# Kernel optimization log

Measured on AMD Instinct MI355X. Metric: run time of the kernel, lower is better.

Reference implementation:

```python
import jax, jax.numpy as jnp
import numpy as np
from jax import lax

D_TEMPORAL, D_INNER, D_STATE, D_CONV, DT_RANK = 2, 4, 16, 4, 1
EPS = 1e-5


def setup_inputs() -> dict:
    key = jax.random.key(0)
    ks = jax.random.split(key, 14)
    B, L = 16, 32768
    f = lambda k, s, scale=1.0: jax.random.normal(k, s, jnp.float32) * scale
    dt_b = float(np.log(np.expm1(0.01)))  # softplus^-1(0.01), typical dt init
    A_log = jnp.log(jnp.tile(jnp.arange(1, D_STATE + 1, dtype=jnp.float32), (D_INNER, 1)))
    return {
        "hidden_states": f(ks[0], (B, D_TEMPORAL, L)),
        "norm_w": jnp.ones((D_TEMPORAL,), jnp.float32),
        "in_proj_w": f(ks[1], (2 * D_INNER, D_TEMPORAL), 0.5),
        "conv_w": f(ks[2], (D_INNER, D_CONV), 0.3),
        "conv_b": f(ks[3], (D_INNER,), 0.1),
        "x_proj_w": f(ks[4], (DT_RANK + 2 * D_STATE, D_INNER), 0.3),
        "dt_proj_w": f(ks[5], (D_INNER, DT_RANK), 1.0),
        "dt_proj_b": jnp.full((D_INNER,), dt_b, jnp.float32),
        "A_log": A_log,
        "D": jnp.ones((D_INNER,), jnp.float32),
        "conv_w_b": f(ks[6], (D_INNER, D_CONV), 0.3),
        "conv_b_b": f(ks[7], (D_INNER,), 0.1),
        "x_proj_w_b": f(ks[8], (DT_RANK + 2 * D_STATE, D_INNER), 0.3),
        "dt_proj_w_b": f(ks[9], (D_INNER, DT_RANK), 1.0),
        "dt_proj_b_b": jnp.full((D_INNER,), dt_b, jnp.float32),
        "A_b_log": A_log,
        "D_b": jnp.ones((D_INNER,), jnp.float32),
        "out_proj_w": f(ks[10], (D_TEMPORAL, D_INNER), 0.3),
        "norm_f_w": jnp.ones((D_TEMPORAL,), jnp.float32),
    }


def _silu(x):
    return x * jax.nn.sigmoid(x)


def _rmsnorm(x, w):
    return x * lax.rsqrt(jnp.mean(x * x, axis=-1, keepdims=True) + EPS) * w


def _branch(x, z, conv_w, conv_b, x_proj_w, dt_proj_w, dt_proj_b, A_log, D):
    # x, z: (B, d_inner, L). Causal depthwise conv + silu.
    Bb, d, L = x.shape
    xc = lax.conv_general_dilated(
        x, conv_w[:, None, :], (1,), [(D_CONV - 1, 0)],
        feature_group_count=d, dimension_numbers=("NCH", "OIH", "NCH"))
    u = _silu(xc + conv_b[None, :, None]).transpose(0, 2, 1)      # (B, L, d)
    x_dbl = u @ x_proj_w.T                                        # (B, L, rank+2n)
    dt, Bm, Cm = jnp.split(x_dbl, [DT_RANK, DT_RANK + D_STATE], axis=-1)
    dt = jax.nn.softplus(dt @ dt_proj_w.T + dt_proj_b)            # (B, L, d)
    A = -jnp.exp(A_log)                                           # (d, n)
    dA = jnp.exp(dt[..., None] * A)                               # (B, L, d, n)
    dBu = (dt * u)[..., None] * Bm[:, :, None, :]                 # (B, L, d, n)

    def step(h, inp):
        dA_t, dBu_t, C_t = inp
        h = dA_t * h + dBu_t                                      # (B, d, n)
        return h, jnp.einsum("bdn,bn->bd", h, C_t)

    h0 = jnp.zeros((Bb, d, D_STATE), dtype=u.dtype)
    _, ys = lax.scan(step, h0, (jnp.swapaxes(dA, 0, 1), jnp.swapaxes(dBu, 0, 1), jnp.swapaxes(Cm, 0, 1)))
    y = jnp.swapaxes(ys, 0, 1) + u * D                            # (B, L, d)
    return y * _silu(z.transpose(0, 2, 1))


def _forward(hidden_states, norm_w, in_proj_w, conv_w, conv_b, x_proj_w, dt_proj_w,
             dt_proj_b, A_log, D, conv_w_b, conv_b_b, x_proj_w_b, dt_proj_w_b,
             dt_proj_b_b, A_b_log, D_b, out_proj_w, norm_f_w):
    # hidden_states: (B, T=d_temporal, L); scan runs over L.
    hs = jnp.swapaxes(hidden_states, 1, 2)                        # (B, L, T)
    residual = hs.astype(jnp.float32)
    hs = _rmsnorm(residual, norm_w)
    xz = jnp.swapaxes(hs @ in_proj_w.T, 1, 2)                     # (B, 2*d_inner, L)
    x, z = jnp.split(xz, 2, axis=1)
    y_f = _branch(x, z, conv_w, conv_b, x_proj_w, dt_proj_w, dt_proj_b, A_log, D)
    y_b = _branch(x[..., ::-1], z[..., ::-1], conv_w_b, conv_b_b, x_proj_w_b,
                  dt_proj_w_b, dt_proj_b_b, A_b_log, D_b)
    y = y_f + y_b[:, ::-1, :]                                     # (B, L, d_inner)
    out = y @ out_proj_w.T                                        # (B, L, T)
    out = _rmsnorm(out + residual, norm_f_w)
    return jnp.swapaxes(out, 1, 2)                                # (B, T, L)


def reference(hidden_states, norm_w, in_proj_w, conv_w, conv_b, x_proj_w, dt_proj_w,
              dt_proj_b, A_log, D, conv_w_b, conv_b_b, x_proj_w_b, dt_proj_w_b,
              dt_proj_b_b, A_b_log, D_b, out_proj_w, norm_f_w):
    return _forward(hidden_states, norm_w, in_proj_w, conv_w, conv_b, x_proj_w,
                    dt_proj_w, dt_proj_b, A_log, D, conv_w_b, conv_b_b, x_proj_w_b,
                    dt_proj_w_b, dt_proj_b_b, A_b_log, D_b, out_proj_w, norm_f_w)
```

## Files before the change

### kernel.cpp

```cpp
#include <hip/hip_runtime.h>
#include <hip/hip_bf16.h>
#include <cstdint>

#define BB 16
#define LL 32768
#define NC 512

#define WD_SZ 256
#define XPW 0
#define CVW 132
#define CVB 148
#define DTW 152
#define DTB 156
#define AW  160
#define DW  224
#define G_INPROJ 512
#define G_NORMW 528
#define G_OUTP 530
#define G_NORMF 538
#define FLG 1000

#define PQ_OFF 4096
#define PQ_BYTES ((size_t)BB*2*NC*64*8)
#define HIN_OFF (PQ_OFF + PQ_BYTES)
#define HIN_BYTES ((size_t)BB*2*NC*64*4)
#define PLN_OFF (HIN_OFF + HIN_BYTES)
#define PLN_STRIDE 14336
#define PLN_BYTES ((size_t)BB*NC*PLN_STRIDE)

#define O_DTF 0
#define O_DTB 1088
#define O_DUF 2176
#define O_DUB 2752
#define O_BCF 3328
#define O_BCB 7680
#define O_ZS  12032
#define O_UD  13056

__device__ __forceinline__ float bf2f(unsigned short u){ return __uint_as_float(((unsigned int)u)<<16); }
__device__ __forceinline__ float blo(unsigned int u){ return __uint_as_float(u<<16); }
__device__ __forceinline__ float bhi(unsigned int u){ return __uint_as_float(u & 0xffff0000u); }
__device__ __forceinline__ unsigned short f2bf(float f){
  unsigned int x = __float_as_uint(f);
  x += 0x7fffu + ((x>>16)&1u);
  return (unsigned short)(x>>16);
}
__device__ __forceinline__ unsigned int pack2(float a, float b){
  __hip_bfloat162 h = __float22bfloat162_rn(make_float2(a,b));
  union { __hip_bfloat162 h2; unsigned int u; } cv; cv.h2 = h;
  return cv.u;
}
__device__ __forceinline__ float siluf(float x){
  return x * __builtin_amdgcn_rcpf(1.f + __expf(-x));
}
__device__ __forceinline__ float softplusf_(float x){
  return fmaxf(x,0.f) + 0.69314718056f*__log2f(1.f + __expf(-fabsf(x)));
}

__device__ __forceinline__ float rowsum16(float x){
  union { float f; int i; } a, t;
  a.f = x;
  t.i = __builtin_amdgcn_update_dpp(0, a.i, 0x121, 0xf, 0xf, true); a.f += t.f;
  t.i = __builtin_amdgcn_update_dpp(0, a.i, 0x122, 0xf, 0xf, true); a.f += t.f;
  t.i = __builtin_amdgcn_update_dpp(0, a.i, 0x124, 0xf, 0xf, true); a.f += t.f;
  t.i = __builtin_amdgcn_update_dpp(0, a.i, 0x128, 0xf, 0xf, true); a.f += t.f;
  return a.f;
}

__device__ __forceinline__ float ldw(const void* p, int i, int isf){
  return isf ? ((const float*)p)[i] : bf2f(((const unsigned short*)p)[i]);
}
__device__ __forceinline__ float2 hid2(const void* hid, int isf, int b, int t){
  if (isf){
    const float* p = (const float*)hid;
    return make_float2(p[(size_t)b*2*LL + t], p[(size_t)b*2*LL + LL + t]);
  }
  const unsigned short* p = (const unsigned short*)hid;
  return make_float2(bf2f(p[(size_t)b*2*LL + t]), bf2f(p[(size_t)b*2*LL + LL + t]));
}
__device__ __forceinline__ float4 xrow(const void* __restrict__ hid, int isf,
                                       const float* __restrict__ W, int b, int t){
  float2 h = hid2(hid, isf, b, t);
  float ms = rsqrtf(0.5f*(h.x*h.x + h.y*h.y) + 1e-5f);
  float v0 = h.x*ms*W[G_NORMW], v1 = h.y*ms*W[G_NORMW+1];
  float4 x;
  x.x = W[G_INPROJ+0]*v0 + W[G_INPROJ+1]*v1;
  x.y = W[G_INPROJ+2]*v0 + W[G_INPROJ+3]*v1;
  x.z = W[G_INPROJ+4]*v0 + W[G_INPROJ+5]*v1;
  x.w = W[G_INPROJ+6]*v0 + W[G_INPROJ+7]*v1;
  return x;
}

__device__ __forceinline__ void phaseA(const void* __restrict__ hid, int isf,
    const float* __restrict__ W, int b, int c, int lane,
    unsigned char* smem, float4* xb)
{
  float* dtF = (float*)(smem+O_DTF);
  float* dtB = (float*)(smem+O_DTB);
  unsigned short* duF = (unsigned short*)(smem+O_DUF);
  unsigned short* duB = (unsigned short*)(smem+O_DUB);
  unsigned int* BCF = (unsigned int*)(smem+O_BCF);
  unsigned int* BCB = (unsigned int*)(smem+O_BCB);
  float* zsP = (float*)(smem+O_ZS);
  float* uDP = (float*)(smem+O_UD);
  {
    int t = c*64 + lane;
    float2 h = hid2(hid, isf, b, t);
    float ms = rsqrtf(0.5f*(h.x*h.x + h.y*h.y) + 1e-5f);
    float v0 = h.x*ms*W[G_NORMW], v1 = h.y*ms*W[G_NORMW+1];
    float4 x;
    x.x = W[G_INPROJ+0]*v0 + W[G_INPROJ+1]*v1;
    x.y = W[G_INPROJ+2]*v0 + W[G_INPROJ+3]*v1;
    x.z = W[G_INPROJ+4]*v0 + W[G_INPROJ+5]*v1;
    x.w = W[G_INPROJ+6]*v0 + W[G_INPROJ+7]*v1;
    xb[lane+3] = x;
    float4 z4;
    z4.x = siluf(W[G_INPROJ+ 8]*v0 + W[G_INPROJ+ 9]*v1);
    z4.y = siluf(W[G_INPROJ+10]*v0 + W[G_INPROJ+11]*v1);
    z4.z = siluf(W[G_INPROJ+12]*v0 + W[G_INPROJ+13]*v1);
    z4.w = siluf(W[G_INPROJ+14]*v0 + W[G_INPROJ+15]*v1);
    *(float4*)&zsP[lane*4] = z4;
    if (lane < 3){
      int t2 = c*64 - 3 + lane;
      float4 v = make_float4(0.f,0.f,0.f,0.f);
      if (t2 >= 0) v = xrow(hid, isf, W, b, t2);
      xb[lane] = v;
    }
    if (lane >= 61){
      int t3 = c*64 + lane + 3;
      float4 v = make_float4(0.f,0.f,0.f,0.f);
      if (t3 < LL) v = xrow(hid, isf, W, b, t3);
      xb[lane+6] = v;
    }
  }
  __syncthreads();
  float4 xk0=xb[lane],xk1=xb[lane+1],xk2=xb[lane+2],xk3=xb[lane+3];
  float4 xk4=xb[lane+4],xk5=xb[lane+5],xk6=xb[lane+6];
  float uf[4], ub[4];
  uf[0] = siluf(W[CVB+0] + W[CVW+ 0]*xk0.x + W[CVW+ 1]*xk1.x + W[CVW+ 2]*xk2.x + W[CVW+ 3]*xk3.x);
  uf[1] = siluf(W[CVB+1] + W[CVW+ 4]*xk0.y + W[CVW+ 5]*xk1.y + W[CVW+ 6]*xk2.y + W[CVW+ 7]*xk3.y);
  uf[2] = siluf(W[CVB+2] + W[CVW+ 8]*xk0.z + W[CVW+ 9]*xk1.z + W[CVW+10]*xk2.z + W[CVW+11]*xk3.z);
  uf[3] = siluf(W[CVB+3] + W[CVW+12]*xk0.w + W[CVW+13]*xk1.w + W[CVW+14]*xk2.w + W[CVW+15]*xk3.w);
  const float* Wb = W + WD_SZ;
  ub[0] = siluf(Wb[CVB+0] + Wb[CVW+ 0]*xk6.x + Wb[CVW+ 1]*xk5.x + Wb[CVW+ 2]*xk4.x + Wb[CVW+ 3]*xk3.x);
  ub[1] = siluf(Wb[CVB+1] + Wb[CVW+ 4]*xk6.y + Wb[CVW+ 5]*xk5.y + Wb[CVW+ 6]*xk4.y + Wb[CVW+ 7]*xk3.y);
  ub[2] = siluf(Wb[CVB+2] + Wb[CVW+ 8]*xk6.z + Wb[CVW+ 9]*xk5.z + Wb[CVW+10]*xk4.z + Wb[CVW+11]*xk3.z);
  ub[3] = siluf(Wb[CVB+3] + Wb[CVW+12]*xk6.w + Wb[CVW+13]*xk5.w + Wb[CVW+14]*xk4.w + Wb[CVW+15]*xk3.w);
  *(float4*)&uDP[lane*4] = make_float4(
      uf[0]*W[DW+0]+ub[0]*Wb[DW+0], uf[1]*W[DW+1]+ub[1]*Wb[DW+1],
      uf[2]*W[DW+2]+ub[2]*Wb[DW+2], uf[3]*W[DW+3]+ub[3]*Wb[DW+3]);
  #pragma unroll
  for (int dr=0; dr<2; dr++){
    const float* Wd = W + dr*WD_SZ;
    const float* uu = dr ? ub : uf;
    float* dtp = dr ? dtB : dtF;
    unsigned short* dup = dr ? duB : duF;
    unsigned int* bcp = dr ? BCB : BCF;
    float dtr = Wd[XPW+0]*uu[0]+Wd[XPW+1]*uu[1]+Wd[XPW+2]*uu[2]+Wd[XPW+3]*uu[3];
    #pragma unroll
    for (int d2=0; d2<4; d2++){
      float dt = softplusf_(fmaf(Wd[DTW+d2], dtr, Wd[DTB+d2]));
      dtp[d2*68+lane] = dt;
      dup[d2*72+lane] = f2bf(dt*uu[d2]);
    }
    #pragma unroll
    for (int n=0;n<16;n++){
      float Bn = Wd[XPW+(1+n)*4+0]*uu[0]+Wd[XPW+(1+n)*4+1]*uu[1]
               + Wd[XPW+(1+n)*4+2]*uu[2]+Wd[XPW+(1+n)*4+3]*uu[3];
      float Cn = Wd[XPW+(17+n)*4+0]*uu[0]+Wd[XPW+(17+n)*4+1]*uu[1]
               + Wd[XPW+(17+n)*4+2]*uu[2]+Wd[XPW+(17+n)*4+3]*uu[3];
      bcp[n*68+lane] = pack2(Bn,Cn);
    }
  }
}

__global__ void k_prep(const void* __restrict__ normw, const void* __restrict__ inpj,
    const void* __restrict__ cwf, const void* __restrict__ cbf,
    const void* __restrict__ xpf, const void* __restrict__ dwf,
    const void* __restrict__ dbf, const void* __restrict__ alf,
    const void* __restrict__ ddf,
    const void* __restrict__ cwb, const void* __restrict__ cbb,
    const void* __restrict__ xpb, const void* __restrict__ dwb,
    const void* __restrict__ dbb, const void* __restrict__ alb,
    const void* __restrict__ ddb,
    const void* __restrict__ outp, const void* __restrict__ nfw,
    float* __restrict__ W)
{
  const int isf = (((const unsigned int*)ddf)[0] == 0x3F800000u) ? 1 : 0;
  int t = threadIdx.x;
  for (int i=t;i<132;i+=256){ W[XPW+i]=ldw(xpf,i,isf); W[WD_SZ+XPW+i]=ldw(xpb,i,isf); }
  for (int i=t;i<16;i+=256){ W[CVW+i]=ldw(cwf,i,isf); W[WD_SZ+CVW+i]=ldw(cwb,i,isf); W[G_INPROJ+i]=ldw(inpj,i,isf); }
  for (int i=t;i<4;i+=256){
    W[CVB+i]=ldw(cbf,i,isf); W[WD_SZ+CVB+i]=ldw(cbb,i,isf);
    W[DTW+i]=ldw(dwf,i,isf); W[WD_SZ+DTW+i]=ldw(dwb,i,isf);
    W[DTB+i]=ldw(dbf,i,isf); W[WD_SZ+DTB+i]=ldw(dbb,i,isf);
    W[DW+i] =ldw(ddf,i,isf); W[WD_SZ+DW+i] =ldw(ddb,i,isf);
  }
  for (int i=t;i<64;i+=256){
    W[AW+i]       = -__expf(ldw(alf,i,isf)) * 1.44269504089f;
    W[WD_SZ+AW+i] = -__expf(ldw(alb,i,isf)) * 1.44269504089f;
  }
  for (int i=t;i<8;i+=256) W[G_OUTP+i]=ldw(outp,i,isf);
  for (int i=t;i<2;i+=256){ W[G_NORMW+i]=ldw(normw,i,isf); W[G_NORMF+i]=ldw(nfw,i,isf); }
  if (t==0) W[FLG] = (float)isf;
}

template<bool SPL>
__global__ __launch_bounds__(64) void k_chunk(const void* __restrict__ hid,
    const float* __restrict__ W, float2* __restrict__ PQ,
    unsigned char* __restrict__ planes)
{
  __shared__ __align__(16) unsigned char smem[PLN_STRIDE];
  __shared__ __align__(16) float4 xb[70];
  const int lane = threadIdx.x;
  const int gid  = blockIdx.x;
  const int c    = gid & (NC-1);
  const int b    = gid >> 9;
  const int isf  = (int)W[FLG];

  phaseA(hid, isf, W, b, c, lane, smem, xb);
  __syncthreads();
  if (SPL){
    uint4* gp = (uint4*)(planes + (size_t)gid*PLN_STRIDE);
    const uint4* sp = (const uint4*)smem;
    #pragma unroll
    for (int i=0;i<14;i++) gp[i*64+lane] = sp[i*64+lane];
  }
  const float* dtF = (const float*)(smem+O_DTF);
  const float* dtB = (const float*)(smem+O_DTB);
  const unsigned short* duF = (const unsigned short*)(smem+O_DUF);
  const unsigned short* duB = (const unsigned short*)(smem+O_DUB);
  const unsigned int* BCF = (const unsigned int*)(smem+O_BCF);
  const unsigned int* BCB = (const unsigned int*)(smem+O_BCB);
  const int d = lane>>4, n = lane&15;
  const float Af = W[AW + d*16 + n];
  const float Ab = W[WD_SZ + AW + d*16 + n];
  float Pf=1.f, Qf=0.f, Pb=1.f, Qb=0.f;
  for (int j4=0; j4<16; j4++){
    const int t0f = j4*4, t0b = 60 - j4*4;
    float4 df4 = *(const float4*)&dtF[d*68+t0f];
    float4 db4 = *(const float4*)&dtB[d*68+t0b];
    uint2 uf2 = *(const uint2*)&duF[d*72+t0f];
    uint2 ub2 = *(const uint2*)&duB[d*72+t0b];
    uint4 cf4 = *(const uint4*)&BCF[n*68+t0f];
    uint4 cb4 = *(const uint4*)&BCB[n*68+t0b];
    float dfa[4]={df4.x,df4.y,df4.z,df4.w}, dba[4]={db4.x,db4.y,db4.z,db4.w};
    float duf[4]={blo(uf2.x),bhi(uf2.x),blo(uf2.y),bhi(uf2.y)};
    float dub[4]={blo(ub2.x),bhi(ub2.x),blo(ub2.y),bhi(ub2.y)};
    unsigned int cfa[4]={cf4.x,cf4.y,cf4.z,cf4.w}, cba[4]={cb4.x,cb4.y,cb4.z,cb4.w};
    #pragma unroll
    for (int jr=0; jr<4; jr++){
      float e = exp2f(Af*dfa[jr]);
      Pf *= e;
      Qf = fmaf(Qf, e, duf[jr]*blo(cfa[jr]));
      const int k = 3-jr;
      float eb = exp2f(Ab*dba[k]);
      Pb *= eb;
      Qb = fmaf(Qb, eb, dub[k]*blo(cba[k]));
    }
  }
  PQ[((size_t)(b*2+0)*NC + c)*64 + lane]        = make_float2(Pf,Qf);
  PQ[((size_t)(b*2+1)*NC + (NC-1-c))*64 + lane] = make_float2(Pb,Qb);
}

__global__ __launch_bounds__(256) void k_scan(const float2* __restrict__ PQ, float* __restrict__ hin)
{
  __shared__ float2 seg[4][64];
  const int bd = blockIdx.x;
  const int lane = threadIdx.x & 63;
  const int w = threadIdx.x >> 6;
  const size_t base = (size_t)bd*NC;
  const int c0 = w*128;
  float h = 0.f, R = 1.f;
  for (int cc=0; cc<128; cc+=16){
    float2 v[16];
    #pragma unroll
    for (int k=0;k<16;k++) v[k] = PQ[(base+c0+cc+k)*64+lane];
    #pragma unroll
    for (int k=0;k<16;k++){
      hin[(base+c0+cc+k)*64+lane] = h;
      h = fmaf(v[k].x, h, v[k].y);
      R *= v[k].x;
    }
  }
  seg[w][lane] = make_float2(R, h);
  __syncthreads();
  if (w > 0){
    float init = 0.f;
    #pragma unroll
    for (int s=0; s<3; s++){
      if (s < w){ float2 pq = seg[s][lane]; init = fmaf(pq.x, init, pq.y); }
    }
    float Rr = 1.f;
    for (int cc=0; cc<128; cc+=16){
      float pv[16], hv[16];
      #pragma unroll
      for (int k=0;k<16;k++) pv[k] = PQ[(base+c0+cc+k)*64+lane].x;
      #pragma unroll
      for (int k=0;k<16;k++) hv[k] = hin[(base+c0+cc+k)*64+lane];
      #pragma unroll
      for (int k=0;k<16;k++){
        hin[(base+c0+cc+k)*64+lane] = hv[k] + init*Rr;
        Rr *= pv[k];
      }
    }
  }
}

template<bool LPL>
__global__ __launch_bounds__(64) void k_fused(const void* __restrict__ hid,
    const float* __restrict__ W, const float* __restrict__ hin,
    const unsigned char* __restrict__ planes, void* __restrict__ out)
{
  __shared__ __align__(16) unsigned char smem[PLN_STRIDE];
  __shared__ __align__(16) float ySf[4][68];
  __shared__ __align__(16) float ySb[4][68];
  const int lane = threadIdx.x;
  const int gid  = blockIdx.x;
  const int c    = gid & (NC-1);
  const int b    = gid >> 9;
  const int isf  = (int)W[FLG];

  float hF = hin[((size_t)(b*2+0)*NC + c)*64 + lane];
  float hB = hin[((size_t)(b*2+1)*NC + (NC-1-c))*64 + lane];

  if constexpr (LPL){
    const uint4* gp = (const uint4*)(planes + (size_t)gid*PLN_STRIDE);
    uint4* sp = (uint4*)smem;
    #pragma unroll
    for (int i=0;i<14;i++) sp[i*64+lane] = gp[i*64+lane];
  } else {
    __shared__ __align__(16) float4 xb[70];
    phaseA(hid, isf, W, b, c, lane, smem, xb);
  }
  __syncthreads();

  const float* dtF = (const float*)(smem+O_DTF);
  const float* dtB = (const float*)(smem+O_DTB);
  const unsigned short* duF = (const unsigned short*)(smem+O_DUF);
  const unsigned short* duB = (const unsigned short*)(smem+O_DUB);
  const unsigned int* BCF = (const unsigned int*)(smem+O_BCF);
  const unsigned int* BCB = (const unsigned int*)(smem+O_BCB);
  const float* zsP = (const float*)(smem+O_ZS);
  const float* uDP = (const float*)(smem+O_UD);

  const int d = lane>>4, n = lane&15;
  const float Af = W[AW + d*16 + n];
  const float Ab = W[WD_SZ + AW + d*16 + n];
  for (int j4=0; j4<16; j4++){
    const int t0f = j4*4, t0b = 60 - j4*4;
    float4 df4 = *(const float4*)&dtF[d*68+t0f];
    float4 db4 = *(const float4*)&dtB[d*68+t0b];
    uint2 uf2 = *(const uint2*)&duF[d*72+t0f];
    uint2 ub2 = *(const uint2*)&duB[d*72+t0b];
    uint4 cf4 = *(const uint4*)&BCF[n*68+t0f];
    uint4 cb4 = *(const uint4*)&BCB[n*68+t0b];
    float dfa[4]={df4.x,df4.y,df4.z,df4.w}, dba[4]={db4.x,db4.y,db4.z,db4.w};
    float duf[4]={blo(uf2.x),bhi(uf2.x),blo(uf2.y),bhi(uf2.y)};
    float dub[4]={blo(ub2.x),bhi(ub2.x),blo(ub2.y),bhi(ub2.y)};
    unsigned int cfa[4]={cf4.x,cf4.y,cf4.z,cf4.w}, cba[4]={cb4.x,cb4.y,cb4.z,cb4.w};
    float sF[4], sB[4];
    #pragma unroll
    for (int jr=0; jr<4; jr++){
      float e = exp2f(Af*dfa[jr]);
      hF = fmaf(e, hF, duf[jr]*blo(cfa[jr]));
      sF[jr] = rowsum16(hF*bhi(cfa[jr]));
      const int k = 3-jr;
      float eb = exp2f(Ab*dba[k]);
      hB = fmaf(eb, hB, dub[k]*blo(cba[k]));
      sB[k] = rowsum16(hB*bhi(cba[k]));
    }
    if (n == 0){
      *(float4*)&ySf[d][t0f] = make_float4(sF[0],sF[1],sF[2],sF[3]);
      *(float4*)&ySb[d][t0b] = make_float4(sB[0],sB[1],sB[2],sB[3]);
    }
  }
  __syncthreads();
  {
    int t = c*64 + lane;
    float4 zz = *(const float4*)&zsP[lane*4];
    float4 ud = *(const float4*)&uDP[lane*4];
    float y0 = (ySf[0][lane] + ySb[0][lane] + ud.x) * zz.x;
    float y1 = (ySf[1][lane] + ySb[1][lane] + ud.y) * zz.y;
    float y2 = (ySf[2][lane] + ySb[2][lane] + ud.z) * zz.z;
    float y3 = (ySf[3][lane] + ySb[3][lane] + ud.w) * zz.w;
    float o0 = W[G_OUTP+0]*y0 + W[G_OUTP+1]*y1 + W[G_OUTP+2]*y2 + W[G_OUTP+3]*y3;
    float o1 = W[G_OUTP+4]*y0 + W[G_OUTP+5]*y1 + W[G_OUTP+6]*y2 + W[G_OUTP+7]*y3;
    float2 r = hid2(hid, isf, b, t);
    o0 += r.x;
    o1 += r.y;
    float ms = rsqrtf(0.5f*(o0*o0 + o1*o1) + 1e-5f);
    float e0 = o0*ms*W[G_NORMF], e1 = o1*ms*W[G_NORMF+1];
    size_t i0 = (size_t)b*2*LL + t, i1 = i0 + LL;
    if (isf){
      ((float*)out)[i0] = e0;
      ((float*)out)[i1] = e1;
    } else {
      ((unsigned short*)out)[i0] = f2bf(e0);
      ((unsigned short*)out)[i1] = f2bf(e1);
    }
  }
}

extern "C" void kernel_launch(void* const* d_in, const int* in_sizes, int n_in,
                              void* d_out, int out_size, void* d_ws, size_t ws_size,
                              hipStream_t stream)
{
  (void)in_sizes; (void)n_in; (void)out_size;
  const void* hid   = d_in[0];
  float* W   = (float*)d_ws;
  float2* PQ = (float2*)((char*)d_ws + PQ_OFF);
  float* hin = (float*)((char*)d_ws + HIN_OFF);
  unsigned char* planes = (unsigned char*)d_ws + PLN_OFF;

  k_prep<<<1,256,0,stream>>>(d_in[1], d_in[2], d_in[3], d_in[4], d_in[5], d_in[6],
                             d_in[7], d_in[8], d_in[9], d_in[10], d_in[11], d_in[12],
                             d_in[13], d_in[14], d_in[15], d_in[16], d_in[17], d_in[18], W);
  const bool useP = ws_size >= (size_t)(PLN_OFF + PLN_BYTES);
  if (useP){
    k_chunk<true><<<BB*NC, 64, 0, stream>>>(hid, W, PQ, planes);
    k_scan<<<BB*2, 256, 0, stream>>>(PQ, hin);
    k_fused<true><<<BB*NC, 64, 0, stream>>>(hid, W, hin, planes, d_out);
  } else {
    k_chunk<false><<<BB*NC, 64, 0, stream>>>(hid, W, PQ, planes);
    k_scan<<<BB*2, 256, 0, stream>>>(PQ, hin);
    k_fused<false><<<BB*NC, 64, 0, stream>>>(hid, W, hin, planes, d_out);
  }
}
```

Baseline: 207.4 us.

## Recompute chunk projections in fused kernel instead of spilling planes to memory

New measurement: 213.2 us. 2.8% more time.

```diff
diff --git a/kernel.cpp b/kernel.cpp
--- a/kernel.cpp
+++ b/kernel.cpp
@@ -23,19 +23,6 @@
 #define PQ_OFF 4096
 #define PQ_BYTES ((size_t)BB*2*NC*64*8)
 #define HIN_OFF (PQ_OFF + PQ_BYTES)
-#define HIN_BYTES ((size_t)BB*2*NC*64*4)
-#define PLN_OFF (HIN_OFF + HIN_BYTES)
-#define PLN_STRIDE 14336
-#define PLN_BYTES ((size_t)BB*NC*PLN_STRIDE)
-
-#define O_DTF 0
-#define O_DTB 1088
-#define O_DUF 2176
-#define O_DUB 2752
-#define O_BCF 3328
-#define O_BCB 7680
-#define O_ZS  12032
-#define O_UD  13056
 
 __device__ __forceinline__ float bf2f(unsigned short u){ return __uint_as_float(((unsigned int)u)<<16); }
 __device__ __forceinline__ float blo(unsigned int u){ return __uint_as_float(u<<16); }
@@ -56,7 +43,6 @@
 __device__ __forceinline__ float softplusf_(float x){
   return fmaxf(x,0.f) + 0.69314718056f*__log2f(1.f + __expf(-fabsf(x)));
 }
-
 __device__ __forceinline__ float rowsum16(float x){
   union { float f; int i; } a, t;
   a.f = x;
@@ -66,7 +52,6 @@
   t.i = __builtin_amdgcn_update_dpp(0, a.i, 0x128, 0xf, 0xf, true); a.f += t.f;
   return a.f;
 }
-
 __device__ __forceinline__ float ldw(const void* p, int i, int isf){
   return isf ? ((const float*)p)[i] : bf2f(((const unsigned short*)p)[i]);
 }
@@ -89,89 +74,6 @@
   x.z = W[G_INPROJ+4]*v0 + W[G_INPROJ+5]*v1;
   x.w = W[G_INPROJ+6]*v0 + W[G_INPROJ+7]*v1;
   return x;
-}
-
-__device__ __forceinline__ void phaseA(const void* __restrict__ hid, int isf,
-    const float* __restrict__ W, int b, int c, int lane,
-    unsigned char* smem, float4* xb)
-{
-  float* dtF = (float*)(smem+O_DTF);
-  float* dtB = (float*)(smem+O_DTB);
-  unsigned short* duF = (unsigned short*)(smem+O_DUF);
-  unsigned short* duB = (unsigned short*)(smem+O_DUB);
-  unsigned int* BCF = (unsigned int*)(smem+O_BCF);
-  unsigned int* BCB = (unsigned int*)(smem+O_BCB);
-  float* zsP = (float*)(smem+O_ZS);
-  float* uDP = (float*)(smem+O_UD);
-  {
-    int t = c*64 + lane;
-    float2 h = hid2(hid, isf, b, t);
-    float ms = rsqrtf(0.5f*(h.x*h.x + h.y*h.y) + 1e-5f);
-    float v0 = h.x*ms*W[G_NORMW], v1 = h.y*ms*W[G_NORMW+1];
-    float4 x;
-    x.x = W[G_INPROJ+0]*v0 + W[G_INPROJ+1]*v1;
-    x.y = W[G_INPROJ+2]*v0 + W[G_INPROJ+3]*v1;
-    x.z = W[G_INPROJ+4]*v0 + W[G_INPROJ+5]*v1;
-    x.w = W[G_INPROJ+6]*v0 + W[G_INPROJ+7]*v1;
-    xb[lane+3] = x;
-    float4 z4;
-    z4.x = siluf(W[G_INPROJ+ 8]*v0 + W[G_INPROJ+ 9]*v1);
-    z4.y = siluf(W[G_INPROJ+10]*v0 + W[G_INPROJ+11]*v1);
-    z4.z = siluf(W[G_INPROJ+12]*v0 + W[G_INPROJ+13]*v1);
-    z4.w = siluf(W[G_INPROJ+14]*v0 + W[G_INPROJ+15]*v1);
-    *(float4*)&zsP[lane*4] = z4;
-    if (lane < 3){
-      int t2 = c*64 - 3 + lane;
-      float4 v = make_float4(0.f,0.f,0.f,0.f);
-      if (t2 >= 0) v = xrow(hid, isf, W, b, t2);
-      xb[lane] = v;
-    }
-    if (lane >= 61){
-      int t3 = c*64 + lane + 3;
-      float4 v = make_float4(0.f,0.f,0.f,0.f);
-      if (t3 < LL) v = xrow(hid, isf, W, b, t3);
-      xb[lane+6] = v;
-    }
-  }
-  __syncthreads();
-  float4 xk0=xb[lane],xk1=xb[lane+1],xk2=xb[lane+2],xk3=xb[lane+3];
-  float4 xk4=xb[lane+4],xk5=xb[lane+5],xk6=xb[lane+6];
-  float uf[4], ub[4];
-  uf[0] = siluf(W[CVB+0] + W[CVW+ 0]*xk0.x + W[CVW+ 1]*xk1.x + W[CVW+ 2]*xk2.x + W[CVW+ 3]*xk3.x);
-  uf[1] = siluf(W[CVB+1] + W[CVW+ 4]*xk0.y + W[CVW+ 5]*xk1.y + W[CVW+ 6]*xk2.y + W[CVW+ 7]*xk3.y);
-  uf[2] = siluf(W[CVB+2] + W[CVW+ 8]*xk0.z + W[CVW+ 9]*xk1.z + W[CVW+10]*xk2.z + W[CVW+11]*xk3.z);
-  uf[3] = siluf(W[CVB+3] + W[CVW+12]*xk0.w + W[CVW+13]*xk1.w + W[CVW+14]*xk2.w + W[CVW+15]*xk3.w);
-  const float* Wb = W + WD_SZ;
-  ub[0] = siluf(Wb[CVB+0] + Wb[CVW+ 0]*xk6.x + Wb[CVW+ 1]*xk5.x + Wb[CVW+ 2]*xk4.x + Wb[CVW+ 3]*xk3.x);
-  ub[1] = siluf(Wb[CVB+1] + Wb[CVW+ 4]*xk6.y + Wb[CVW+ 5]*xk5.y + Wb[CVW+ 6]*xk4.y + Wb[CVW+ 7]*xk3.y);
-  ub[2] = siluf(Wb[CVB+2] + Wb[CVW+ 8]*xk6.z + Wb[CVW+ 9]*xk5.z + Wb[CVW+10]*xk4.z + Wb[CVW+11]*xk3.z);
-  ub[3] = siluf(Wb[CVB+3] + Wb[CVW+12]*xk6.w + Wb[CVW+13]*xk5.w + Wb[CVW+14]*xk4.w + Wb[CVW+15]*xk3.w);
-  *(float4*)&uDP[lane*4] = make_float4(
-      uf[0]*W[DW+0]+ub[0]*Wb[DW+0], uf[1]*W[DW+1]+ub[1]*Wb[DW+1],
-      uf[2]*W[DW+2]+ub[2]*Wb[DW+2], uf[3]*W[DW+3]+ub[3]*Wb[DW+3]);
-  #pragma unroll
-  for (int dr=0; dr<2; dr++){
-    const float* Wd = W + dr*WD_SZ;
-    const float* uu = dr ? ub : uf;
-    float* dtp = dr ? dtB : dtF;
-    unsigned short* dup = dr ? duB : duF;
-    unsigned int* bcp = dr ? BCB : BCF;
-    float dtr = Wd[XPW+0]*uu[0]+Wd[XPW+1]*uu[1]+Wd[XPW+2]*uu[2]+Wd[XPW+3]*uu[3];
-    #pragma unroll
-    for (int d2=0; d2<4; d2++){
-      float dt = softplusf_(fmaf(Wd[DTW+d2], dtr, Wd[DTB+d2]));
-      dtp[d2*68+lane] = dt;
-      dup[d2*72+lane] = f2bf(dt*uu[d2]);
-    }
-    #pragma unroll
-    for (int n=0;n<16;n++){
-      float Bn = Wd[XPW+(1+n)*4+0]*uu[0]+Wd[XPW+(1+n)*4+1]*uu[1]
-               + Wd[XPW+(1+n)*4+2]*uu[2]+Wd[XPW+(1+n)*4+3]*uu[3];
-      float Cn = Wd[XPW+(17+n)*4+0]*uu[0]+Wd[XPW+(17+n)*4+1]*uu[1]
-               + Wd[XPW+(17+n)*4+2]*uu[2]+Wd[XPW+(17+n)*4+3]*uu[3];
-      bcp[n*68+lane] = pack2(Bn,Cn);
-    }
-  }
 }
 
 __global__ void k_prep(const void* __restrict__ normw, const void* __restrict__ inpj,
@@ -205,74 +107,105 @@
   if (t==0) W[FLG] = (float)isf;
 }
 
-template<bool SPL>
-__global__ __launch_bounds__(64) void k_chunk(const void* __restrict__ hid,
-    const float* __restrict__ W, float2* __restrict__ PQ,
-    unsigned char* __restrict__ planes)
+__global__ __launch_bounds__(128) void k_chunk(const void* __restrict__ hid,
+    const float* __restrict__ W, float2* __restrict__ PQ)
 {
-  __shared__ __align__(16) unsigned char smem[PLN_STRIDE];
-  __shared__ __align__(16) float4 xb[70];
-  const int lane = threadIdx.x;
-  const int gid  = blockIdx.x;
+  __shared__ __align__(16) unsigned int   DUc[2][2][4*68];
+  __shared__ __align__(16) unsigned short Bsc[2][2][16*72];
+  __shared__ __align__(16) float4 xbc[2][70];
+  const int lane = threadIdx.x & 63;
+  const int w    = threadIdx.x >> 6;
+  const int gid  = blockIdx.x*2 + w;
   const int c    = gid & (NC-1);
   const int b    = gid >> 9;
   const int isf  = (int)W[FLG];
 
-  phaseA(hid, isf, W, b, c, lane, smem, xb);
-  __syncthreads();
-  if (SPL){
-    uint4* gp = (uint4*)(planes + (size_t)gid*PLN_STRIDE);
-    const uint4* sp = (const uint4*)smem;
-    #pragma unroll
-    for (int i=0;i<14;i++) gp[i*64+lane] = sp[i*64+lane];
-  }
-  const float* dtF = (const float*)(smem+O_DTF);
-  const float* dtB = (const float*)(smem+O_DTB);
-  const unsigned short* duF = (const unsigned short*)(smem+O_DUF);
-  const unsigned short* duB = (const unsigned short*)(smem+O_DUB);
-  const unsigned int* BCF = (const unsigned int*)(smem+O_BCF);
-  const unsigned int* BCB = (const unsigned int*)(smem+O_BCB);
+  {
+    int t = c*64 + lane;
+    xbc[w][lane+3] = xrow(hid, isf, W, b, t);
+    if (lane < 3){
+      int t2 = c*64 - 3 + lane;
+      float4 v = make_float4(0.f,0.f,0.f,0.f);
+      if (t2 >= 0) v = xrow(hid, isf, W, b, t2);
+      xbc[w][lane] = v;
+    }
+    if (lane >= 61){
+      int t3 = c*64 + lane + 3;
+      float4 v = make_float4(0.f,0.f,0.f,0.f);
+      if (t3 < LL) v = xrow(hid, isf, W, b, t3);
+      xbc[w][lane+6] = v;
+    }
+  }
+  __syncthreads();
+  {
+    float4 xk0=xbc[w][lane],xk1=xbc[w][lane+1],xk2=xbc[w][lane+2],xk3=xbc[w][lane+3];
+    float4 xk4=xbc[w][lane+4],xk5=xbc[w][lane+5],xk6=xbc[w][lane+6];
+    float uf[4], ub[4];
+    uf[0] = siluf(W[CVB+0] + W[CVW+ 0]*xk0.x + W[CVW+ 1]*xk1.x + W[CVW+ 2]*xk2.x + W[CVW+ 3]*xk3.x);
+    uf[1] = siluf(W[CVB+1] + W[CVW+ 4]*xk0.y + W[CVW+ 5]*xk1.y + W[CVW+ 6]*xk2.y + W[CVW+ 7]*xk3.y);
+    uf[2] = siluf(W[CVB+2] + W[CVW+ 8]*xk0.z + W[CVW+ 9]*xk1.z + W[CVW+10]*xk2.z + W[CVW+11]*xk3.z);
+    uf[3] = siluf(W[CVB+3] + W[CVW+12]*xk0.w + W[CVW+13]*xk1.w + W[CVW+14]*xk2.w + W[CVW+15]*xk3.w);
+    const float* Wb = W + WD_SZ;
+    ub[0] = siluf(Wb[CVB+0] + Wb[CVW+ 0]*xk6.x + Wb[CVW+ 1]*xk5.x + Wb[CVW+ 2]*xk4.x + Wb[CVW+ 3]*xk3.x);
+    ub[1] = siluf(Wb[CVB+1] + Wb[CVW+ 4]*xk6.y + Wb[CVW+ 5]*xk5.y + Wb[CVW+ 6]*xk4.y + Wb[CVW+ 7]*xk3.y);
+    ub[2] = siluf(Wb[CVB+2] + Wb[CVW+ 8]*xk6.z + Wb[CVW+ 9]*xk5.z + Wb[CVW+10]*xk4.z + Wb[CVW+11]*xk3.z);
+    ub[3] = siluf(Wb[CVB+3] + Wb[CVW+12]*xk6.w + Wb[CVW+13]*xk5.w + Wb[CVW+14]*xk4.w + Wb[CVW+15]*xk3.w);
+    #pragma unroll
+    for (int dr=0; dr<2; dr++){
+      const float* Wd = W + dr*WD_SZ;
+      const float* uu = dr ? ub : uf;
+      float dtr = Wd[XPW+0]*uu[0]+Wd[XPW+1]*uu[1]+Wd[XPW+2]*uu[2]+Wd[XPW+3]*uu[3];
+      #pragma unroll
+      for (int d2=0; d2<4; d2++){
+        float dt = softplusf_(fmaf(Wd[DTW+d2], dtr, Wd[DTB+d2]));
+        DUc[w][dr][d2*68+lane] = pack2(dt, dt*uu[d2]);
+      }
+      #pragma unroll
+      for (int n=0;n<16;n++){
+        float Bn = Wd[XPW+(1+n)*4+0]*uu[0]+Wd[XPW+(1+n)*4+1]*uu[1]
+                 + Wd[XPW+(1+n)*4+2]*uu[2]+Wd[XPW+(1+n)*4+3]*uu[3];
+        Bsc[w][dr][n*72+lane] = f2bf(Bn);
+      }
+    }
+  }
+  __syncthreads();
   const int d = lane>>4, n = lane&15;
   const float Af = W[AW + d*16 + n];
   const float Ab = W[WD_SZ + AW + d*16 + n];
   float Pf=1.f, Qf=0.f, Pb=1.f, Qb=0.f;
   for (int j4=0; j4<16; j4++){
     const int t0f = j4*4, t0b = 60 - j4*4;
-    float4 df4 = *(const float4*)&dtF[d*68+t0f];
-    float4 db4 = *(const float4*)&dtB[d*68+t0b];
-    uint2 uf2 = *(const uint2*)&duF[d*72+t0f];
-    uint2 ub2 = *(const uint2*)&duB[d*72+t0b];
-    uint4 cf4 = *(const uint4*)&BCF[n*68+t0f];
-    uint4 cb4 = *(const uint4*)&BCB[n*68+t0b];
-    float dfa[4]={df4.x,df4.y,df4.z,df4.w}, dba[4]={db4.x,db4.y,db4.z,db4.w};
-    float duf[4]={blo(uf2.x),bhi(uf2.x),blo(uf2.y),bhi(uf2.y)};
-    float dub[4]={blo(ub2.x),bhi(ub2.x),blo(ub2.y),bhi(ub2.y)};
-    unsigned int cfa[4]={cf4.x,cf4.y,cf4.z,cf4.w}, cba[4]={cb4.x,cb4.y,cb4.z,cb4.w};
+    uint4 uf4 = *(const uint4*)&DUc[w][0][d*68+t0f];
+    uint4 ub4 = *(const uint4*)&DUc[w][1][d*68+t0b];
+    ushort4 bf4 = *(const ushort4*)&Bsc[w][0][n*72+t0f];
+    ushort4 bb4 = *(const ushort4*)&Bsc[w][1][n*72+t0b];
+    unsigned int ufa[4]={uf4.x,uf4.y,uf4.z,uf4.w}, uba[4]={ub4.x,ub4.y,ub4.z,ub4.w};
+    unsigned short bfa[4]={bf4.x,bf4.y,bf4.z,bf4.w}, bba[4]={bb4.x,bb4.y,bb4.z,bb4.w};
     #pragma unroll
     for (int jr=0; jr<4; jr++){
-      float e = exp2f(Af*dfa[jr]);
+      float e = exp2f(Af*blo(ufa[jr]));
       Pf *= e;
-      Qf = fmaf(Qf, e, duf[jr]*blo(cfa[jr]));
+      Qf = fmaf(Qf, e, bhi(ufa[jr])*bf2f(bfa[jr]));
       const int k = 3-jr;
-      float eb = exp2f(Ab*dba[k]);
+      float eb = exp2f(Ab*blo(uba[k]));
       Pb *= eb;
-      Qb = fmaf(Qb, eb, dub[k]*blo(cba[k]));
+      Qb = fmaf(Qb, eb, bhi(uba[k])*bf2f(bba[k]));
     }
   }
   PQ[((size_t)(b*2+0)*NC + c)*64 + lane]        = make_float2(Pf,Qf);
   PQ[((size_t)(b*2+1)*NC + (NC-1-c))*64 + lane] = make_float2(Pb,Qb);
 }
 
-__global__ __launch_bounds__(256) void k_scan(const float2* __restrict__ PQ, float* __restrict__ hin)
+__global__ __launch_bounds__(512) void k_scan(const float2* __restrict__ PQ, float* __restrict__ hin)
 {
-  __shared__ float2 seg[4][64];
+  __shared__ float2 seg[8][64];
   const int bd = blockIdx.x;
   const int lane = threadIdx.x & 63;
   const int w = threadIdx.x >> 6;
   const size_t base = (size_t)bd*NC;
-  const int c0 = w*128;
+  const int c0 = w*64;
   float h = 0.f, R = 1.f;
-  for (int cc=0; cc<128; cc+=16){
+  for (int cc=0; cc<64; cc+=16){
     float2 v[16];
     #pragma unroll
     for (int k=0;k<16;k++) v[k] = PQ[(base+c0+cc+k)*64+lane];
@@ -288,11 +221,11 @@
   if (w > 0){
     float init = 0.f;
     #pragma unroll
-    for (int s=0; s<3; s++){
+    for (int s=0; s<7; s++){
       if (s < w){ float2 pq = seg[s][lane]; init = fmaf(pq.x, init, pq.y); }
     }
     float Rr = 1.f;
-    for (int cc=0; cc<128; cc+=16){
+    for (int cc=0; cc<64; cc+=16){
       float pv[16], hv[16];
       #pragma unroll
       for (int k=0;k<16;k++) pv[k] = PQ[(base+c0+cc+k)*64+lane].x;
@@ -307,16 +240,19 @@
   }
 }
 
-template<bool LPL>
-__global__ __launch_bounds__(64) void k_fused(const void* __restrict__ hid,
+__global__ __launch_bounds__(128) void k_fused(const void* __restrict__ hid,
     const float* __restrict__ W, const float* __restrict__ hin,
-    const unsigned char* __restrict__ planes, void* __restrict__ out)
+    void* __restrict__ out)
 {
-  __shared__ __align__(16) unsigned char smem[PLN_STRIDE];
-  __shared__ __align__(16) float ySf[4][68];
-  __shared__ __align__(16) float ySb[4][68];
-  const int lane = threadIdx.x;
-  const int gid  = blockIdx.x;
+  __shared__ __align__(16) unsigned int DUf[2][2][4*68];
+  __shared__ __align__(16) unsigned int BCf[2][2][16*68];
+  __shared__ __align__(16) float4 xbf[2][70];
+  __shared__ __align__(16) float zsf[2][256];
+  __shared__ __align__(16) float uDf[2][256];
+  __shared__ __align__(16) float ySm[2][256];
+  const int lane = threadIdx.x & 63;
+  const int w    = threadIdx.x >> 6;
+  const int gid  = blockIdx.x*2 + w;
   const int c    = gid & (NC-1);
   const int b    = gid >> 9;
   const int isf  = (int)W[FLG];
@@ -324,66 +260,125 @@
   float hF = hin[((size_t)(b*2+0)*NC + c)*64 + lane];
   float hB = hin[((size_t)(b*2+1)*NC + (NC-1-c))*64 + lane];
 
-  if constexpr (LPL){
-    const uint4* gp = (const uint4*)(planes + (size_t)gid*PLN_STRIDE);
-    uint4* sp = (uint4*)smem;
-    #pragma unroll
-    for (int i=0;i<14;i++) sp[i*64+lane] = gp[i*64+lane];
-  } else {
-    __shared__ __align__(16) float4 xb[70];
-    phaseA(hid, isf, W, b, c, lane, smem, xb);
-  }
-  __syncthreads();
-
-  const float* dtF = (const float*)(smem+O_DTF);
-  const float* dtB = (const float*)(smem+O_DTB);
-  const unsigned short* duF = (const unsigned short*)(smem+O_DUF);
-  const unsigned short* duB = (const unsigned short*)(smem+O_DUB);
-  const unsigned int* BCF = (const unsigned int*)(smem+O_BCF);
-  const unsigned int* BCB = (const unsigned int*)(smem+O_BCB);
-  const float* zsP = (const float*)(smem+O_ZS);
-  const float* uDP = (const float*)(smem+O_UD);
+  {
+    int t = c*64 + lane;
+    float2 h = hid2(hid, isf, b, t);
+    float ms = rsqrtf(0.5f*(h.x*h.x + h.y*h.y) + 1e-5f);
+    float v0 = h.x*ms*W[G_NORMW], v1 = h.y*ms*W[G_NORMW+1];
+    float4 x;
+    x.x = W[G_INPROJ+0]*v0 + W[G_INPROJ+1]*v1;
+    x.y = W[G_INPROJ+2]*v0 + W[G_INPROJ+3]*v1;
+    x.z = W[G_INPROJ+4]*v0 + W[G_INPROJ+5]*v1;
+    x.w = W[G_INPROJ+6]*v0 + W[G_INPROJ+7]*v1;
+    xbf[w][lane+3] = x;
+    float4 z4;
+    z4.x = siluf(W[G_INPROJ+ 8]*v0 + W[G_INPROJ+ 9]*v1);
+    z4.y = siluf(W[G_INPROJ+10]*v0 + W[G_INPROJ+11]*v1);
+    z4.z = siluf(W[G_INPROJ+12]*v0 + W[G_INPROJ+13]*v1);
+    z4.w = siluf(W[G_INPROJ+14]*v0 + W[G_INPROJ+15]*v1);
+    *(float4*)&zsf[w][lane*4] = z4;
+    if (lane < 3){
+      int t2 = c*64 - 3 + lane;
+      float4 v = make_float4(0.f,0.f,0.f,0.f);
+      if (t2 >= 0) v = xrow(hid, isf, W, b, t2);
+      xbf[w][lane] = v;
+    }
+    if (lane >= 61){
+      int t3 = c*64 + lane + 3;
+      float4 v = make_float4(0.f,0.f,0.f,0.f);
+      if (t3 < LL) v = xrow(hid, isf, W, b, t3);
+      xbf[w][lane+6] = v;
+    }
+  }
+  __syncthreads();
+  {
+    float4 xk0=xbf[w][lane],xk1=xbf[w][lane+1],xk2=xbf[w][lane+2],xk3=xbf[w][lane+3];
+    float4 xk4=xbf[w][lane+4],xk5=xbf[w][lane+5],xk6=xbf[w][lane+6];
+    float uf[4], ub[4];
+    uf[0] = siluf(W[CVB+0] + W[CVW+ 0]*xk0.x + W[CVW+ 1]*xk1.x + W[CVW+ 2]*xk2.x + W[CVW+ 3]*xk3.x);
+    uf[1] = siluf(W[CVB+1] + W[CVW+ 4]*xk0.y + W[CVW+ 5]*xk1.y + W[CVW+ 6]*xk2.y + W[CVW+ 7]*xk3.y);
+    uf[2] = siluf(W[CVB+2] + W[CVW+ 8]*xk0.z + W[CVW+ 9]*xk1.z + W[CVW+10]*xk2.z + W[CVW+11]*xk3.z);
+    uf[3] = siluf(W[CVB+3] + W[CVW+12]*xk0.w + W[CVW+13]*xk1.w + W[CVW+14]*xk2.w + W[CVW+15]*xk3.w);
+    const float* Wb = W + WD_SZ;
+    ub[0] = siluf(Wb[CVB+0] + Wb[CVW+ 0]*xk6.x + Wb[CVW+ 1]*xk5.x + Wb[CVW+ 2]*xk4.x + Wb[CVW+ 3]*xk3.x);
+    ub[1] = siluf(Wb[CVB+1] + Wb[CVW+ 4]*xk6.y + Wb[CVW+ 5]*xk5.y + Wb[CVW+ 6]*xk4.y + Wb[CVW+ 7]*xk3.y);
+    ub[2] = siluf(Wb[CVB+2] + Wb[CVW+ 8]*xk6.z + Wb[CVW+ 9]*xk5.z + Wb[CVW+10]*xk4.z + Wb[CVW+11]*xk3.z);
+    ub[3] = siluf(Wb[CVB+3] + Wb[CVW+12]*xk6.w + Wb[CVW+13]*xk5.w + Wb[CVW+14]*xk4.w + Wb[CVW+15]*xk3.w);
+    *(float4*)&uDf[w][lane*4] = make_float4(
+        uf[0]*W[DW+0]+ub[0]*Wb[DW+0], uf[1]*W[DW+1]+ub[1]*Wb[DW+1],
+        uf[2]*W[DW+2]+ub[2]*Wb[DW+2], uf[3]*W[DW+3]+ub[3]*Wb[DW+3]);
+    #pragma unroll
+    for (int dr=0; dr<2; dr++){
+      const float* Wd = W + dr*WD_SZ;
+      const float* uu = dr ? ub : uf;
+      float dtr = Wd[XPW+0]*uu[0]+Wd[XPW+1]*uu[1]+Wd[XPW+2]*uu[2]+Wd[XPW+3]*uu[3];
+      #pragma unroll
+      for (int d2=0; d2<4; d2++){
+        float dt = softplusf_(fmaf(Wd[DTW+d2], dtr, Wd[DTB+d2]));
+        DUf[w][dr][d2*68+lane] = pack2(dt, dt*uu[d2]);
+      }
+      #pragma unroll
+      for (int n=0;n<16;n++){
+        float Bn = Wd[XPW+(1+n)*4+0]*uu[0]+Wd[XPW+(1+n)*4+1]*uu[1]
+                 + Wd[XPW+(1+n)*4+2]*uu[2]+Wd[XPW+(1+n)*4+3]*uu[3];
+        float Cn = Wd[XPW+(17+n)*4+0]*uu[0]+Wd[XPW+(17+n)*4+1]*uu[1]
+                 + Wd[XPW+(17+n)*4+2]*uu[2]+Wd[XPW+(17+n)*4+3]*uu[3];
+        BCf[w][dr][n*68+lane] = pack2(Bn,Cn);
+      }
+    }
+  }
+  __syncthreads();
 
   const int d = lane>>4, n = lane&15;
-  const float Af = W[AW + d*16 + n];
-  const float Ab = W[WD_SZ + AW + d*16 + n];
-  for (int j4=0; j4<16; j4++){
-    const int t0f = j4*4, t0b = 60 - j4*4;
-    float4 df4 = *(const float4*)&dtF[d*68+t0f];
-    float4 db4 = *(const float4*)&dtB[d*68+t0b];
-    uint2 uf2 = *(const uint2*)&duF[d*72+t0f];
-    uint2 ub2 = *(const uint2*)&duB[d*72+t0b];
-    uint4 cf4 = *(const uint4*)&BCF[n*68+t0f];
-    uint4 cb4 = *(const uint4*)&BCB[n*68+t0b];
-    float dfa[4]={df4.x,df4.y,df4.z,df4.w}, dba[4]={db4.x,db4.y,db4.z,db4.w};
-    float duf[4]={blo(uf2.x),bhi(uf2.x),blo(uf2.y),bhi(uf2.y)};
-    float dub[4]={blo(ub2.x),bhi(ub2.x),blo(ub2.y),bhi(ub2.y)};
-    unsigned int cfa[4]={cf4.x,cf4.y,cf4.z,cf4.w}, cba[4]={cb4.x,cb4.y,cb4.z,cb4.w};
-    float sF[4], sB[4];
-    #pragma unroll
-    for (int jr=0; jr<4; jr++){
-      float e = exp2f(Af*dfa[jr]);
-      hF = fmaf(e, hF, duf[jr]*blo(cfa[jr]));
-      sF[jr] = rowsum16(hF*bhi(cfa[jr]));
-      const int k = 3-jr;
-      float eb = exp2f(Ab*dba[k]);
-      hB = fmaf(eb, hB, dub[k]*blo(cba[k]));
-      sB[k] = rowsum16(hB*bhi(cba[k]));
-    }
-    if (n == 0){
-      *(float4*)&ySf[d][t0f] = make_float4(sF[0],sF[1],sF[2],sF[3]);
-      *(float4*)&ySb[d][t0b] = make_float4(sB[0],sB[1],sB[2],sB[3]);
+  {
+    const float Af = W[AW + d*16 + n];
+    for (int j4=0; j4<16; j4++){
+      const int t0 = j4*4;
+      uint4 u4 = *(const uint4*)&DUf[w][0][d*68+t0];
+      uint4 c4 = *(const uint4*)&BCf[w][0][n*68+t0];
+      unsigned int ua[4]={u4.x,u4.y,u4.z,u4.w};
+      unsigned int ca[4]={c4.x,c4.y,c4.z,c4.w};
+      float s[4];
+      #pragma unroll
+      for (int jr=0; jr<4; jr++){
+        float e = exp2f(Af*blo(ua[jr]));
+        hF = fmaf(e, hF, bhi(ua[jr])*blo(ca[jr]));
+        s[jr] = rowsum16(hF*bhi(ca[jr]));
+      }
+      if (n == 0) *(float4*)&ySm[w][d*64+t0] = make_float4(s[0],s[1],s[2],s[3]);
+    }
+  }
+  {
+    const float Ab = W[WD_SZ + AW + d*16 + n];
+    for (int j4=0; j4<16; j4++){
+      const int t0 = 60 - j4*4;
+      uint4 u4 = *(const uint4*)&DUf[w][1][d*68+t0];
+      uint4 c4 = *(const uint4*)&BCf[w][1][n*68+t0];
+      unsigned int ua[4]={u4.x,u4.y,u4.z,u4.w};
+      unsigned int ca[4]={c4.x,c4.y,c4.z,c4.w};
+      float s[4];
+      #pragma unroll
+      for (int jr=0; jr<4; jr++){
+        const int k = 3-jr;
+        float e = exp2f(Ab*blo(ua[k]));
+        hB = fmaf(e, hB, bhi(ua[k])*blo(ca[k]));
+        s[k] = rowsum16(hB*bhi(ca[k]));
+      }
+      if (n == 0){
+        float4 f = *(const float4*)&ySm[w][d*64+t0];
+        *(float4*)&ySm[w][d*64+t0] = make_float4(f.x+s[0],f.y+s[1],f.z+s[2],f.w+s[3]);
+      }
     }
   }
   __syncthreads();
   {
     int t = c*64 + lane;
-    float4 zz = *(const float4*)&zsP[lane*4];
-    float4 ud = *(const float4*)&uDP[lane*4];
-    float y0 = (ySf[0][lane] + ySb[0][lane] + ud.x) * zz.x;
-    float y1 = (ySf[1][lane] + ySb[1][lane] + ud.y) * zz.y;
-    float y2 = (ySf[2][lane] + ySb[2][lane] + ud.z) * zz.z;
-    float y3 = (ySf[3][lane] + ySb[3][lane] + ud.w) * zz.w;
+    float4 zz = *(const float4*)&zsf[w][lane*4];
+    float4 ud = *(const float4*)&uDf[w][lane*4];
+    float y0 = (ySm[w][0*64+lane] + ud.x) * zz.x;
+    float y1 = (ySm[w][1*64+lane] + ud.y) * zz.y;
+    float y2 = (ySm[w][2*64+lane] + ud.z) * zz.z;
+    float y3 = (ySm[w][3*64+lane] + ud.w) * zz.w;
     float o0 = W[G_OUTP+0]*y0 + W[G_OUTP+1]*y1 + W[G_OUTP+2]*y2 + W[G_OUTP+3]*y3;
     float o1 = W[G_OUTP+4]*y0 + W[G_OUTP+5]*y1 + W[G_OUTP+6]*y2 + W[G_OUTP+7]*y3;
     float2 r = hid2(hid, isf, b, t);
@@ -406,24 +401,16 @@
                               void* d_out, int out_size, void* d_ws, size_t ws_size,
                               hipStream_t stream)
 {
-  (void)in_sizes; (void)n_in; (void)out_size;
-  const void* hid   = d_in[0];
+  (void)in_sizes; (void)n_in; (void)out_size; (void)ws_size;
+  const void* hid = d_in[0];
   float* W   = (float*)d_ws;
   float2* PQ = (float2*)((char*)d_ws + PQ_OFF);
   float* hin = (float*)((char*)d_ws + HIN_OFF);
-  unsigned char* planes = (unsigned char*)d_ws + PLN_OFF;
 
   k_prep<<<1,256,0,stream>>>(d_in[1], d_in[2], d_in[3], d_in[4], d_in[5], d_in[6],
                              d_in[7], d_in[8], d_in[9], d_in[10], d_in[11], d_in[12],
                              d_in[13], d_in[14], d_in[15], d_in[16], d_in[17], d_in[18], W);
-  const bool useP = ws_size >= (size_t)(PLN_OFF + PLN_BYTES);
-  if (useP){
-    k_chunk<true><<<BB*NC, 64, 0, stream>>>(hid, W, PQ, planes);
-    k_scan<<<BB*2, 256, 0, stream>>>(PQ, hin);
-    k_fused<true><<<BB*NC, 64, 0, stream>>>(hid, W, hin, planes, d_out);
-  } else {
-    k_chunk<false><<<BB*NC, 64, 0, stream>>>(hid, W, PQ, planes);
-    k_scan<<<BB*2, 256, 0, stream>>>(PQ, hin);
-    k_fused<false><<<BB*NC, 64, 0, stream>>>(hid, W, hin, planes, d_out);
-  }
-}
+  k_chunk<<<BB*NC/2, 128, 0, stream>>>(hid, W, PQ);
+  k_scan<<<BB*2, 512, 0, stream>>>(PQ, hin);
+  k_fused<<<BB*NC/2, 128, 0, stream>>>(hid, W, hin, d_out);
+}
```
